# Optimization experiments

Hardware: AMD Instinct MI355X
Metric: run time of the kernel (lower is better)

Reference implementation:

```python
import jax, jax.numpy as jnp
import numpy as np

D_MODEL = 1024
N_HEADS = 16
D_FF = 4096
WINDOW = 256
EPS = 1e-5


def setup_inputs() -> dict:
    key = jax.random.key(0)
    ks = jax.random.split(key, 12)
    B, T, C = 4, 1024, D_MODEL
    s = lambda fan: 1.0 / np.sqrt(fan)
    return {
        "x": jax.random.normal(ks[0], (B, T, C), jnp.float32),
        "Wqkv": jax.random.normal(ks[1], (3 * C, C), jnp.float32) * s(C),
        "bqkv": jnp.zeros((3 * C,), jnp.float32),
        "Wo": jax.random.normal(ks[2], (C, C), jnp.float32) * s(C),
        "bo": jnp.zeros((C,), jnp.float32),
        "W1": jax.random.normal(ks[3], (D_FF, C), jnp.float32) * s(C),
        "b1": jnp.zeros((D_FF,), jnp.float32),
        "W2": jax.random.normal(ks[4], (C, D_FF), jnp.float32) * s(D_FF),
        "b2": jnp.zeros((C,), jnp.float32),
        "g1": jnp.ones((C,), jnp.float32),
        "be1": jnp.zeros((C,), jnp.float32),
        "g2": jnp.ones((C,), jnp.float32),
        "be2": jnp.zeros((C,), jnp.float32),
    }


def _layernorm(x, g, b):
    mu = jnp.mean(x, axis=-1, keepdims=True)
    var = jnp.mean(jnp.square(x - mu), axis=-1, keepdims=True)
    return (x - mu) * jax.lax.rsqrt(var + EPS) * g + b


def reference(x, Wqkv, bqkv, Wo, bo, W1, b1, W2, b2, g1, be1, g2, be2):
    B, T, C = x.shape
    H, Dh = N_HEADS, C // N_HEADS
    # QKV projection (torch MultiheadAttention packed in_proj)
    qkv = jnp.einsum("btc,ec->bte", x, Wqkv) + bqkv  # [B,T,3C]
    q, k, v = jnp.split(qkv, 3, axis=-1)
    q = q.reshape(B, T, H, Dh).transpose(0, 2, 1, 3)  # [B,H,T,Dh]
    k = k.reshape(B, T, H, Dh).transpose(0, 2, 1, 3)
    v = v.reshape(B, T, H, Dh).transpose(0, 2, 1, 3)
    scores = jnp.einsum("bhqd,bhkd->bhqk", q, k) / jnp.sqrt(jnp.float32(Dh))
    # causal banded mask: key j visible to query i iff 0 <= i-j < WINDOW
    i = jnp.arange(T)[:, None]
    j = jnp.arange(T)[None, :]
    band = (j <= i) & (i - j < WINDOW)
    scores = jnp.where(band, scores, -jnp.inf)
    attn = jax.nn.softmax(scores, axis=-1)
    ctx = jnp.einsum("bhqk,bhkd->bhqd", attn, v)  # [B,H,T,Dh]
    ctx = ctx.transpose(0, 2, 1, 3).reshape(B, T, C)
    attn_out = jnp.einsum("btc,oc->bto", ctx, Wo) + bo
    x = _layernorm(x + attn_out, g1, be1)
    h = jax.nn.gelu(jnp.einsum("btc,fc->btf", x, W1) + b1, approximate=False)
    ffn_out = jnp.einsum("btf,cf->btc", h, W2) + b2
    return _layernorm(x + ffn_out, g2, be2)
```

## Files before the change

kernel.cpp:

```cpp
#include <hip/hip_runtime.h>
#include <hip/hip_bf16.h>

typedef __attribute__((ext_vector_type(4))) float floatx4;
typedef __attribute__((ext_vector_type(8))) short shortx8;

struct bf4 { __hip_bfloat16 h[4]; };
union U8 { shortx8 v; __hip_bfloat16 h[8]; };
union U4 { unsigned long long v; __hip_bfloat16 h[4]; };

__device__ __forceinline__ void async_copy16(const __hip_bfloat16* g, __hip_bfloat16* l) {
  __builtin_amdgcn_global_load_lds((__attribute__((address_space(1))) void*)g,
                                   (__attribute__((address_space(3))) void*)l,
                                   16, 0, 0);
}

__global__ __launch_bounds__(256) void cast_all_kernel(
    const float* __restrict__ s0, __hip_bfloat16* __restrict__ d0, int nb0,
    const float* __restrict__ s1, __hip_bfloat16* __restrict__ d1, int nb1,
    const float* __restrict__ s2, __hip_bfloat16* __restrict__ d2, int nb2,
    const float* __restrict__ s3, __hip_bfloat16* __restrict__ d3, int nb3,
    const float* __restrict__ s4, __hip_bfloat16* __restrict__ d4) {
  int b = blockIdx.x;
  const float* src; __hip_bfloat16* dst;
  if (b < nb0) { src = s0; dst = d0; }
  else { b -= nb0;
    if (b < nb1) { src = s1; dst = d1; }
    else { b -= nb1;
      if (b < nb2) { src = s2; dst = d2; }
      else { b -= nb2;
        if (b < nb3) { src = s3; dst = d3; }
        else { b -= nb3; src = s4; dst = d4; }
      }
    }
  }
  const int i = b * 256 + threadIdx.x;
  const float4 v = ((const float4*)src)[i];
  bf4 o4;
  o4.h[0] = __float2bfloat16(v.x);
  o4.h[1] = __float2bfloat16(v.y);
  o4.h[2] = __float2bfloat16(v.z);
  o4.h[3] = __float2bfloat16(v.w);
  *(bf4*)(dst + (size_t)i * 4) = o4;
}

#define G6_VM(n)   asm volatile("s_waitcnt vmcnt(" #n ")" ::: "memory")
#define G6_BAR()   asm volatile("s_barrier" ::: "memory")
#define G6_LGKM0() asm volatile("s_waitcnt lgkmcnt(0)" ::: "memory")

#define G6_VMSEL(nf, np)                                                       \
  if (NBF == 4 || tid < 256 * NBF) { G6_VM(nf); } else { G6_VM(np); }

#define G6_BSTG(s, off)                                                        \
  if (NBF == 4 || tid < 256 * NBF) {                                           \
    async_copy16(Bg + (off), &Bs[(s) * BSLOT + tid * 8]);                      \
  }

#define G6_KLOOP()                                                             \
  async_copy16(Ag,      &As[0 * 8192 + tid * 8]);                              \
  G6_BSTG(0, 0)                                                                \
  async_copy16(Ag + 32, &As[1 * 8192 + tid * 8]);                              \
  G6_BSTG(1, 32)                                                               \
  async_copy16(Ag + 64, &As[2 * 8192 + tid * 8]);                              \
  G6_BSTG(2, 64)                                                               \
  G6_VMSEL(4, 2); G6_BAR();                                                    \
  {                                                                            \
    int rs = 0, ws = 3, koff = 96;                                             \
    for (int u = 0; u < NH; ++u) {                                             \
      const __hip_bfloat16* Asl = As + rs * 8192;                              \
      const __hip_bfloat16* Bsl = Bs + rs * BSLOT;                             \
      shortx8 fa[4], fb[NBF];                                                  \
      _Pragma("unroll")                                                        \
      for (int i_ = 0; i_ < 4; ++i_)                                           \
        fa[i_] = *(const shortx8*)&Asl[ard + i_ * 512];                        \
      _Pragma("unroll")                                                        \
      for (int i_ = 0; i_ < NBF; ++i_)                                         \
        fb[i_] = *(const shortx8*)&Bsl[brd + i_ * 512];                        \
      if (u + 3 < NH) {                                                        \
        async_copy16(Ag + koff, &As[ws * 8192 + tid * 8]);                     \
        G6_BSTG(ws, koff)                                                      \
        koff += 32;                                                            \
        G6_VMSEL(4, 2);                                                        \
      } else if (u + 2 < NH) { G6_VMSEL(2, 1); }                               \
      else if (u + 1 < NH)   { G6_VMSEL(0, 0); }                               \
      G6_BAR();                                                                \
      G6_LGKM0();                                                              \
      __builtin_amdgcn_s_setprio(1);                                           \
      _Pragma("unroll")                                                        \
      for (int mi_ = 0; mi_ < 4; ++mi_)                                        \
        _Pragma("unroll")                                                      \
        for (int ni_ = 0; ni_ < NBF; ++ni_)                                    \
          acc[mi_][ni_] = __builtin_amdgcn_mfma_f32_16x16x32_bf16(             \
              fa[mi_], fb[ni_], acc[mi_][ni_], 0, 0, 0);                       \
      __builtin_amdgcn_s_setprio(0);                                           \
      rs = (rs == 4) ? 0 : rs + 1;                                             \
      ws = (ws == 4) ? 0 : ws + 1;                                             \
    }                                                                          \
  }

template<int EPI, int NBF>
__global__ __launch_bounds__(1024, 4) void gemm256(
    const __hip_bfloat16* __restrict__ A,
    const __hip_bfloat16* __restrict__ B,
    const float* __restrict__ bias,
    __hip_bfloat16* __restrict__ outb,
    int M, int N, int K, int NT)
{
  __shared__ __align__(16) __hip_bfloat16 As[5 * 8192];
  __shared__ __align__(16) __hip_bfloat16 Bs[5 * 2048 * NBF];
  const int BSLOT = 2048 * NBF;
  const int tid  = threadIdx.x;
  const int lane = tid & 63;
  const int wave = tid >> 6;
  const int wr = wave >> 2;
  const int wc = wave & 3;
  const int fr = lane & 15;
  const int fq = lane >> 4;

  const int nwg = gridDim.x;
  const int cpx = nwg >> 3;
  const int swz = (blockIdx.x & 7) * cpx + (blockIdx.x >> 3);
  const int mt = swz / NT, nt = swz % NT;
  const long bm = (long)mt * 256, bn = (long)nt * (64 * NBF);

  const int srow = tid >> 2;
  const int sch  = (tid & 3) ^ ((tid >> 3) & 3);
  const __hip_bfloat16* Ag = A + (bm + srow) * (size_t)K + sch * 8;
  const __hip_bfloat16* Bg = B + (bn + srow) * (size_t)K + sch * 8;

  const int swc = (fq ^ ((fr >> 1) & 3)) << 3;
  const int ard = (wr * 64 + fr) * 32 + swc;
  const int brd = (wc * (16 * NBF) + fr) * 32 + swc;

  const floatx4 zero = {0.f, 0.f, 0.f, 0.f};
  floatx4 acc[4][NBF];
#pragma unroll
  for (int mi = 0; mi < 4; ++mi)
#pragma unroll
    for (int ni = 0; ni < NBF; ++ni) acc[mi][ni] = zero;

  const int NH = K >> 5;
  G6_KLOOP()

#pragma unroll
  for (int mi = 0; mi < 4; ++mi) {
#pragma unroll
    for (int ni = 0; ni < NBF; ++ni) {
      const long col = bn + wc * (16 * NBF) + ni * 16 + fr;
      const float bv = bias[col];
#pragma unroll
      for (int r = 0; r < 4; ++r) {
        const long row = bm + wr * 64 + mi * 16 + fq * 4 + r;
        float v = acc[mi][ni][r] + bv;
        if (EPI == 1) {
          const float u = v + 0.044715f * v * v * v;
          v = v / (1.0f + __expf(-1.5957691216057308f * u));
        }
        outb[(size_t)row * N + col] = __float2bfloat16(v);
      }
    }
  }
}

__global__ __launch_bounds__(1024, 4) void gemm256_splitk(
    const __hip_bfloat16* __restrict__ A,
    const __hip_bfloat16* __restrict__ B,
    __hip_bfloat16* __restrict__ part,
    int M, int N, int K, int Klen, int NT, int TPS)
{
  __shared__ __align__(16) __hip_bfloat16 As[5 * 8192];
  __shared__ __align__(16) __hip_bfloat16 Bs[5 * 8192];
  const int NBF = 4;
  const int BSLOT = 8192;
  const int tid  = threadIdx.x;
  const int lane = tid & 63;
  const int wave = tid >> 6;
  const int wr = wave >> 2;
  const int wc = wave & 3;
  const int fr = lane & 15;
  const int fq = lane >> 4;

  const int nwg = gridDim.x;
  const int cpx = nwg >> 3;
  const int swz = (blockIdx.x & 7) * cpx + (blockIdx.x >> 3);
  const int zt = swz / TPS;
  const int tile = swz % TPS;
  const int mt = tile / NT, nt = tile % NT;
  const long bm = (long)mt * 256, bn = (long)nt * 256;
  const int kstart = zt * Klen;

  const int srow = tid >> 2;
  const int sch  = (tid & 3) ^ ((tid >> 3) & 3);
  const __hip_bfloat16* Ag = A + (bm + srow) * (size_t)K + kstart + sch * 8;
  const __hip_bfloat16* Bg = B + (bn + srow) * (size_t)K + kstart + sch * 8;

  const int swc = (fq ^ ((fr >> 1) & 3)) << 3;
  const int ard = (wr * 64 + fr) * 32 + swc;
  const int brd = (wc * 64 + fr) * 32 + swc;

  const floatx4 zero = {0.f, 0.f, 0.f, 0.f};
  floatx4 acc[4][4];
#pragma unroll
  for (int mi = 0; mi < 4; ++mi)
#pragma unroll
    for (int ni = 0; ni < 4; ++ni) acc[mi][ni] = zero;

  const int NH = Klen >> 5;
  G6_KLOOP()

  __hip_bfloat16* outp = part + (size_t)zt * M * N;
#pragma unroll
  for (int mi = 0; mi < 4; ++mi) {
#pragma unroll
    for (int ni = 0; ni < 4; ++ni) {
      const long col = bn + wc * 64 + ni * 16 + fr;
#pragma unroll
      for (int r = 0; r < 4; ++r) {
        const long row = bm + wr * 64 + mi * 16 + fq * 4 + r;
        outp[(size_t)row * N + col] = __float2bfloat16(acc[mi][ni][r]);
      }
    }
  }
}

__global__ __launch_bounds__(256) void transpose_v_kernel(
    const __hip_bfloat16* __restrict__ qkv, __hip_bfloat16* __restrict__ vt)
{
  const int bh = blockIdx.y;
  const int tt = blockIdx.x;
  const int b = bh >> 4, h = bh & 15;
  __shared__ __hip_bfloat16 tile[64][65];
  const int tid = threadIdx.x;
  const int r = tid >> 2;
  const int c = (tid & 3) << 4;
  const __hip_bfloat16* src = qkv + (size_t)(b * 1024 + tt * 64 + r) * 3072 + 2048 + h * 64 + c;
  U8 u0, u1;
  u0.v = *(const shortx8*)src;
  u1.v = *(const shortx8*)(src + 8);
#pragma unroll
  for (int j = 0; j < 8; ++j) { tile[r][c + j] = u0.h[j]; tile[r][c + 8 + j] = u1.h[j]; }
  __syncthreads();
  U8 w0, w1;
#pragma unroll
  for (int j = 0; j < 8; ++j) { w0.h[j] = tile[c + j][r]; w1.h[j] = tile[c + 8 + j][r]; }
  __hip_bfloat16* dst = vt + ((size_t)bh * 64 + r) * 1024 + tt * 64 + c;
  *(shortx8*)dst       = w0.v;
  *(shortx8*)(dst + 8) = w1.v;
}

__global__ __launch_bounds__(256) void attn_kernel(
    const __hip_bfloat16* __restrict__ qkv,
    const __hip_bfloat16* __restrict__ vt,
    __hip_bfloat16* __restrict__ ctx)
{
  const int wave = threadIdx.x >> 6;
  const int lane = threadIdx.x & 63;
  const int gw = blockIdx.x * 4 + wave;
  const int qt = gw & 63;
  const int bh = gw >> 6;
  const int b = bh >> 4, h = bh & 15;
  const int fr = lane & 15, fq = lane >> 4;
  const int q0 = qt << 4;

  __shared__ __align__(16) __hip_bfloat16 Plds[4][16 * 32];
  __hip_bfloat16* Pw = Plds[wave];

  const __hip_bfloat16* qrow = qkv + (size_t)(b * 1024 + q0 + fr) * 3072 + h * 64;
  const shortx8 aq0 = *(const shortx8*)(qrow + fq * 8);
  const shortx8 aq1 = *(const shortx8*)(qrow + 32 + fq * 8);

  const float SC = 0.125f * 1.44269504088896f;
  float m_r[4] = {-1e30f, -1e30f, -1e30f, -1e30f};
  float l_r[4] = {0.f, 0.f, 0.f, 0.f};
  const floatx4 zero = {0.f, 0.f, 0.f, 0.f};
  floatx4 o[4];
#pragma unroll
  for (int nd = 0; nd < 4; ++nd) o[nd] = zero;

  const int kt0 = (q0 >= 255) ? ((q0 - 255) >> 5) : 0;
  const int kt1 = (q0 + 15) >> 5;
  for (int kt = kt0; kt <= kt1; ++kt) {
    const int kbase = kt << 5;
    const __hip_bfloat16* krow0 = qkv + (size_t)(b * 1024 + kbase + fr) * 3072 + 1024 + h * 64;
    const __hip_bfloat16* krow1 = krow0 + 16 * 3072;
    const shortx8 bk00 = *(const shortx8*)(krow0 + fq * 8);
    const shortx8 bk01 = *(const shortx8*)(krow0 + 32 + fq * 8);
    const shortx8 bk10 = *(const shortx8*)(krow1 + fq * 8);
    const shortx8 bk11 = *(const shortx8*)(krow1 + 32 + fq * 8);
    floatx4 s0 = zero, s1 = zero;
    s0 = __builtin_amdgcn_mfma_f32_16x16x32_bf16(aq0, bk00, s0, 0, 0, 0);
    s0 = __builtin_amdgcn_mfma_f32_16x16x32_bf16(aq1, bk01, s0, 0, 0, 0);
    s1 = __builtin_amdgcn_mfma_f32_16x16x32_bf16(aq0, bk10, s1, 0, 0, 0);
    s1 = __builtin_amdgcn_mfma_f32_16x16x32_bf16(aq1, bk11, s1, 0, 0, 0);
#pragma unroll
    for (int r = 0; r < 4; ++r) { s0[r] *= SC; s1[r] *= SC; }
    if (kbase + 31 > q0 || kbase < q0 - 240) {
#pragma unroll
      for (int r = 0; r < 4; ++r) {
        const int tq = q0 + fq * 4 + r;
        const int j0 = kbase + fr;
        const int j1 = j0 + 16;
        if (j0 > tq || j0 < tq - 255) s0[r] = -3e38f;
        if (j1 > tq || j1 < tq - 255) s1[r] = -3e38f;
      }
    }
#pragma unroll
    for (int r = 0; r < 4; ++r) {
      float vmax = fmaxf(s0[r], s1[r]);
      vmax = fmaxf(vmax, __shfl_xor(vmax, 1));
      vmax = fmaxf(vmax, __shfl_xor(vmax, 2));
      vmax = fmaxf(vmax, __shfl_xor(vmax, 4));
      vmax = fmaxf(vmax, __shfl_xor(vmax, 8));
      const float mnew = fmaxf(m_r[r], vmax);
      const float alpha = exp2f(m_r[r] - mnew);
      const float p0 = exp2f(s0[r] - mnew);
      const float p1 = exp2f(s1[r] - mnew);
      m_r[r] = mnew;
      float ps = p0 + p1;
      ps += __shfl_xor(ps, 1);
      ps += __shfl_xor(ps, 2);
      ps += __shfl_xor(ps, 4);
      ps += __shfl_xor(ps, 8);
      l_r[r] = l_r[r] * alpha + ps;
      o[0][r] *= alpha; o[1][r] *= alpha; o[2][r] *= alpha; o[3][r] *= alpha;
      Pw[(fq * 4 + r) * 32 + fr]      = __float2bfloat16(p0);
      Pw[(fq * 4 + r) * 32 + 16 + fr] = __float2bfloat16(p1);
    }
    asm volatile("s_waitcnt lgkmcnt(0)" ::: "memory");
    const shortx8 ap = *(const shortx8*)&Pw[fr * 32 + fq * 8];
#pragma unroll
    for (int nd = 0; nd < 4; ++nd) {
      const shortx8 bv = *(const shortx8*)&vt[((size_t)bh * 64 + nd * 16 + fr) * 1024 + kbase + fq * 8];
      o[nd] = __builtin_amdgcn_mfma_f32_16x16x32_bf16(ap, bv, o[nd], 0, 0, 0);
    }
    asm volatile("s_waitcnt lgkmcnt(0)" ::: "memory");
  }
#pragma unroll
  for (int nd = 0; nd < 4; ++nd)
#pragma unroll
    for (int r = 0; r < 4; ++r)
      ctx[(size_t)(b * 1024 + q0 + fq * 4 + r) * 1024 + h * 64 + nd * 16 + fr] =
          __float2bfloat16(o[nd][r] / l_r[r]);
}

template<int S, int WB>
__global__ __launch_bounds__(256) void ln_sum_kernel(
    const __hip_bfloat16* __restrict__ part,
    const float* __restrict__ resid,
    const float* __restrict__ bias,
    const float* __restrict__ g, const float* __restrict__ be,
    float* __restrict__ outf, __hip_bfloat16* __restrict__ outb)
{
  const int row = blockIdx.x;
  const int tid = threadIdx.x;
  const size_t base = (size_t)row * 1024;
  float4 v = ((const float4*)(resid + base))[tid];
  const float4 bv = ((const float4*)bias)[tid];
  v.x += bv.x; v.y += bv.y; v.z += bv.z; v.w += bv.w;
#pragma unroll
  for (int s = 0; s < S; ++s) {
    U4 p;
    p.v = *(const unsigned long long*)&part[(size_t)s * 4096 * 1024 + base + tid * 4];
    v.x += __bfloat162float(p.h[0]);
    v.y += __bfloat162float(p.h[1]);
    v.z += __bfloat162float(p.h[2]);
    v.w += __bfloat162float(p.h[3]);
  }
  float sm = v.x + v.y + v.z + v.w;
  float ss = v.x * v.x + v.y * v.y + v.z * v.z + v.w * v.w;
#pragma unroll
  for (int off = 1; off < 64; off <<= 1) {
    sm += __shfl_xor(sm, off);
    ss += __shfl_xor(ss, off);
  }
  __shared__ float red[8];
  if ((tid & 63) == 0) { red[tid >> 6] = sm; red[4 + (tid >> 6)] = ss; }
  __syncthreads();
  sm = red[0] + red[1] + red[2] + red[3];
  ss = red[4] + red[5] + red[6] + red[7];
  const float mu = sm * (1.0f / 1024.0f);
  const float rs = rsqrtf(ss * (1.0f / 1024.0f) - mu * mu + 1e-5f);
  const float4 gg = ((const float4*)g)[tid];
  const float4 bb = ((const float4*)be)[tid];
  float4 y;
  y.x = (v.x - mu) * rs * gg.x + bb.x;
  y.y = (v.y - mu) * rs * gg.y + bb.y;
  y.z = (v.z - mu) * rs * gg.z + bb.z;
  y.w = (v.w - mu) * rs * gg.w + bb.w;
  ((float4*)(outf + base))[tid] = y;
  if (WB) {
    bf4 o4;
    o4.h[0] = __float2bfloat16(y.x);
    o4.h[1] = __float2bfloat16(y.y);
    o4.h[2] = __float2bfloat16(y.z);
    o4.h[3] = __float2bfloat16(y.w);
    *(bf4*)(outb + base + tid * 4) = o4;
  }
}

extern "C" void kernel_launch(void* const* d_in, const int* in_sizes, int n_in,
                              void* d_out, int out_size, void* d_ws, size_t ws_size,
                              hipStream_t stream) {
  const float* x    = (const float*)d_in[0];
  const float* Wqkv = (const float*)d_in[1];
  const float* bqkv = (const float*)d_in[2];
  const float* Wo   = (const float*)d_in[3];
  const float* bo   = (const float*)d_in[4];
  const float* W1   = (const float*)d_in[5];
  const float* b1   = (const float*)d_in[6];
  const float* W2   = (const float*)d_in[7];
  const float* b2   = (const float*)d_in[8];
  const float* g1   = (const float*)d_in[9];
  const float* be1  = (const float*)d_in[10];
  const float* g2   = (const float*)d_in[11];
  const float* be2  = (const float*)d_in[12];

  char* ws = (char*)d_ws;
  size_t off = 0;
  auto alloc = [&](size_t bytes) -> void* {
    void* p = ws + off;
    off += (bytes + 255) & ~(size_t)255;
    return p;
  };
  __hip_bfloat16* wqkvb = (__hip_bfloat16*)alloc(6291456);
  __hip_bfloat16* wob   = (__hip_bfloat16*)alloc(2097152);
  __hip_bfloat16* w1b   = (__hip_bfloat16*)alloc(8388608);
  __hip_bfloat16* w2b   = (__hip_bfloat16*)alloc(8388608);
  __hip_bfloat16* xb    = (__hip_bfloat16*)alloc(8388608);
  __hip_bfloat16* qkvb  = (__hip_bfloat16*)alloc(25165824);
  __hip_bfloat16* vtb   = (__hip_bfloat16*)alloc(8388608);
  __hip_bfloat16* ctxb  = (__hip_bfloat16*)alloc(8388608);
  __hip_bfloat16* part  = (__hip_bfloat16*)alloc(4u * 8388608);
  float*          x1f   = (float*)alloc(16777216);
  __hip_bfloat16* x1b   = (__hip_bfloat16*)alloc(8388608);
  __hip_bfloat16* hb    = (__hip_bfloat16*)alloc(33554432);
  (void)ws_size; (void)in_sizes; (void)n_in; (void)out_size;

  cast_all_kernel<<<16384, 256, 0, stream>>>(x, xb, 4096,
                                             Wqkv, wqkvb, 3072,
                                             Wo, wob, 1024,
                                             W1, w1b, 4096,
                                             W2, w2b);
  gemm256<0, 3><<<256, 1024, 0, stream>>>(xb, wqkvb, bqkv, qkvb, 4096, 3072, 1024, 16);
  transpose_v_kernel<<<dim3(16, 64), 256, 0, stream>>>(qkvb, vtb);
  attn_kernel<<<1024, 256, 0, stream>>>(qkvb, vtb, ctxb);
  gemm256_splitk<<<256, 1024, 0, stream>>>(ctxb, wob, part, 4096, 1024, 1024, 256, 4, 64);
  ln_sum_kernel<4, 1><<<4096, 256, 0, stream>>>(part, x, bo, g1, be1, x1f, x1b);
  gemm256<1, 4><<<256, 1024, 0, stream>>>(x1b, w1b, b1, hb, 4096, 4096, 1024, 16);
  gemm256_splitk<<<256, 1024, 0, stream>>>(hb, w2b, part, 4096, 1024, 4096, 1024, 4, 64);
  ln_sum_kernel<4, 0><<<4096, 256, 0, stream>>>(part, x1f, b2, g2, be2, (float*)d_out, nullptr);
}
```

Baseline: 323.1 us.

## Software-pipeline K loads and hoist V loads in banded attention loop

The attention loop is manually unrolled by two with ping-pong K register sets, so the next K tile is prefetched while the current tile runs softmax. V fragments are loaded at the top of each step instead of after the P tile is written, so their latency hides behind the QK MFMAs and softmax. The P staging buffer row stride goes from 32 to 40 elements to reduce LDS bank conflicts. In exchange the kernel uses more registers, which may lower occupancy.

```diff
diff --git a/kernel.cpp b/kernel.cpp
--- a/kernel.cpp
+++ b/kernel.cpp
@@ -247,6 +247,74 @@
   *(shortx8*)(dst + 8) = w1.v;
 }
 
+#define ATTN_LOADK(k0, k1, k2, k3, ktv)                                        \
+  {                                                                            \
+    const __hip_bfloat16* kr0_ =                                               \
+        qkv + (size_t)(b * 1024 + ((ktv) << 5) + fr) * 3072 + 1024 + h * 64;   \
+    const __hip_bfloat16* kr1_ = kr0_ + 16 * 3072;                             \
+    k0 = *(const shortx8*)(kr0_ + fq * 8);                                     \
+    k1 = *(const shortx8*)(kr0_ + 32 + fq * 8);                                \
+    k2 = *(const shortx8*)(kr1_ + fq * 8);                                     \
+    k3 = *(const shortx8*)(kr1_ + 32 + fq * 8);                                \
+  }
+
+#define ATTN_STEP(KC0, KC1, KC2, KC3, KN0, KN1, KN2, KN3, ktv, PREF)           \
+  {                                                                            \
+    const int kbase = (ktv) << 5;                                              \
+    const __hip_bfloat16* vrow_ =                                              \
+        vt + ((size_t)bh * 64 + fr) * 1024 + kbase + fq * 8;                   \
+    const shortx8 vv0 = *(const shortx8*)(vrow_);                              \
+    const shortx8 vv1 = *(const shortx8*)(vrow_ + 16 * 1024);                  \
+    const shortx8 vv2 = *(const shortx8*)(vrow_ + 32 * 1024);                  \
+    const shortx8 vv3 = *(const shortx8*)(vrow_ + 48 * 1024);                  \
+    floatx4 s0 = zero, s1 = zero;                                              \
+    s0 = __builtin_amdgcn_mfma_f32_16x16x32_bf16(aq0, KC0, s0, 0, 0, 0);       \
+    s0 = __builtin_amdgcn_mfma_f32_16x16x32_bf16(aq1, KC1, s0, 0, 0, 0);       \
+    s1 = __builtin_amdgcn_mfma_f32_16x16x32_bf16(aq0, KC2, s1, 0, 0, 0);       \
+    s1 = __builtin_amdgcn_mfma_f32_16x16x32_bf16(aq1, KC3, s1, 0, 0, 0);       \
+    if (PREF) ATTN_LOADK(KN0, KN1, KN2, KN3, (ktv) + 1)                        \
+    _Pragma("unroll")                                                          \
+    for (int r = 0; r < 4; ++r) { s0[r] *= SC; s1[r] *= SC; }                  \
+    if (kbase + 31 > q0 || kbase < q0 - 240) {                                 \
+      _Pragma("unroll")                                                        \
+      for (int r = 0; r < 4; ++r) {                                            \
+        const int tq = q0 + fq * 4 + r;                                        \
+        const int j0 = kbase + fr;                                             \
+        const int j1 = j0 + 16;                                                \
+        if (j0 > tq || j0 < tq - 255) s0[r] = -3e38f;                          \
+        if (j1 > tq || j1 < tq - 255) s1[r] = -3e38f;                          \
+      }                                                                        \
+    }                                                                          \
+    _Pragma("unroll")                                                          \
+    for (int r = 0; r < 4; ++r) {                                              \
+      float vmax = fmaxf(s0[r], s1[r]);                                        \
+      vmax = fmaxf(vmax, __shfl_xor(vmax, 1));                                 \
+      vmax = fmaxf(vmax, __shfl_xor(vmax, 2));                                 \
+      vmax = fmaxf(vmax, __shfl_xor(vmax, 4));                                 \
+      vmax = fmaxf(vmax, __shfl_xor(vmax, 8));                                 \
+      const float mnew = fmaxf(m_r[r], vmax);                                  \
+      const float alpha = exp2f(m_r[r] - mnew);                                \
+      const float p0 = exp2f(s0[r] - mnew);                                    \
+      const float p1 = exp2f(s1[r] - mnew);                                    \
+      m_r[r] = mnew;                                                           \
+      float ps = p0 + p1;                                                      \
+      ps += __shfl_xor(ps, 1);                                                 \
+      ps += __shfl_xor(ps, 2);                                                 \
+      ps += __shfl_xor(ps, 4);                                                 \
+      ps += __shfl_xor(ps, 8);                                                 \
+      l_r[r] = l_r[r] * alpha + ps;                                            \
+      o[0][r] *= alpha; o[1][r] *= alpha; o[2][r] *= alpha; o[3][r] *= alpha;  \
+      Pw[(fq * 4 + r) * 40 + fr]      = __float2bfloat16(p0);                  \
+      Pw[(fq * 4 + r) * 40 + 16 + fr] = __float2bfloat16(p1);                  \
+    }                                                                          \
+    asm volatile("s_waitcnt lgkmcnt(0)" ::: "memory");                         \
+    const shortx8 ap = *(const shortx8*)&Pw[fr * 40 + fq * 8];                 \
+    o[0] = __builtin_amdgcn_mfma_f32_16x16x32_bf16(ap, vv0, o[0], 0, 0, 0);    \
+    o[1] = __builtin_amdgcn_mfma_f32_16x16x32_bf16(ap, vv1, o[1], 0, 0, 0);    \
+    o[2] = __builtin_amdgcn_mfma_f32_16x16x32_bf16(ap, vv2, o[2], 0, 0, 0);    \
+    o[3] = __builtin_amdgcn_mfma_f32_16x16x32_bf16(ap, vv3, o[3], 0, 0, 0);    \
+  }
+
 __global__ __launch_bounds__(256) void attn_kernel(
     const __hip_bfloat16* __restrict__ qkv,
     const __hip_bfloat16* __restrict__ vt,
@@ -261,7 +329,7 @@
   const int fr = lane & 15, fq = lane >> 4;
   const int q0 = qt << 4;
 
-  __shared__ __align__(16) __hip_bfloat16 Plds[4][16 * 32];
+  __shared__ __align__(16) __hip_bfloat16 Plds[4][16 * 40];
   __hip_bfloat16* Pw = Plds[wave];
 
   const __hip_bfloat16* qrow = qkv + (size_t)(b * 1024 + q0 + fr) * 3072 + h * 64;
@@ -278,62 +346,21 @@
 
   const int kt0 = (q0 >= 255) ? ((q0 - 255) >> 5) : 0;
   const int kt1 = (q0 + 15) >> 5;
-  for (int kt = kt0; kt <= kt1; ++kt) {
-    const int kbase = kt << 5;
-    const __hip_bfloat16* krow0 = qkv + (size_t)(b * 1024 + kbase + fr) * 3072 + 1024 + h * 64;
-    const __hip_bfloat16* krow1 = krow0 + 16 * 3072;
-    const shortx8 bk00 = *(const shortx8*)(krow0 + fq * 8);
-    const shortx8 bk01 = *(const shortx8*)(krow0 + 32 + fq * 8);
-    const shortx8 bk10 = *(const shortx8*)(krow1 + fq * 8);
-    const shortx8 bk11 = *(const shortx8*)(krow1 + 32 + fq * 8);
-    floatx4 s0 = zero, s1 = zero;
-    s0 = __builtin_amdgcn_mfma_f32_16x16x32_bf16(aq0, bk00, s0, 0, 0, 0);
-    s0 = __builtin_amdgcn_mfma_f32_16x16x32_bf16(aq1, bk01, s0, 0, 0, 0);
-    s1 = __builtin_amdgcn_mfma_f32_16x16x32_bf16(aq0, bk10, s1, 0, 0, 0);
-    s1 = __builtin_amdgcn_mfma_f32_16x16x32_bf16(aq1, bk11, s1, 0, 0, 0);
-#pragma unroll
-    for (int r = 0; r < 4; ++r) { s0[r] *= SC; s1[r] *= SC; }
-    if (kbase + 31 > q0 || kbase < q0 - 240) {
-#pragma unroll
-      for (int r = 0; r < 4; ++r) {
-        const int tq = q0 + fq * 4 + r;
-        const int j0 = kbase + fr;
-        const int j1 = j0 + 16;
-        if (j0 > tq || j0 < tq - 255) s0[r] = -3e38f;
-        if (j1 > tq || j1 < tq - 255) s1[r] = -3e38f;
-      }
-    }
-#pragma unroll
-    for (int r = 0; r < 4; ++r) {
-      float vmax = fmaxf(s0[r], s1[r]);
-      vmax = fmaxf(vmax, __shfl_xor(vmax, 1));
-      vmax = fmaxf(vmax, __shfl_xor(vmax, 2));
-      vmax = fmaxf(vmax, __shfl_xor(vmax, 4));
-      vmax = fmaxf(vmax, __shfl_xor(vmax, 8));
-      const float mnew = fmaxf(m_r[r], vmax);
-      const float alpha = exp2f(m_r[r] - mnew);
-      const float p0 = exp2f(s0[r] - mnew);
-      const float p1 = exp2f(s1[r] - mnew);
-      m_r[r] = mnew;
-      float ps = p0 + p1;
-      ps += __shfl_xor(ps, 1);
-      ps += __shfl_xor(ps, 2);
-      ps += __shfl_xor(ps, 4);
-      ps += __shfl_xor(ps, 8);
-      l_r[r] = l_r[r] * alpha + ps;
-      o[0][r] *= alpha; o[1][r] *= alpha; o[2][r] *= alpha; o[3][r] *= alpha;
-      Pw[(fq * 4 + r) * 32 + fr]      = __float2bfloat16(p0);
-      Pw[(fq * 4 + r) * 32 + 16 + fr] = __float2bfloat16(p1);
-    }
-    asm volatile("s_waitcnt lgkmcnt(0)" ::: "memory");
-    const shortx8 ap = *(const shortx8*)&Pw[fr * 32 + fq * 8];
-#pragma unroll
-    for (int nd = 0; nd < 4; ++nd) {
-      const shortx8 bv = *(const shortx8*)&vt[((size_t)bh * 64 + nd * 16 + fr) * 1024 + kbase + fq * 8];
-      o[nd] = __builtin_amdgcn_mfma_f32_16x16x32_bf16(ap, bv, o[nd], 0, 0, 0);
-    }
-    asm volatile("s_waitcnt lgkmcnt(0)" ::: "memory");
-  }
+
+  shortx8 ka0, ka1, ka2, ka3, kb0, kb1, kb2, kb3;
+  ATTN_LOADK(ka0, ka1, ka2, ka3, kt0)
+  int kt = kt0;
+  for (;;) {
+    const bool more1 = kt < kt1;
+    ATTN_STEP(ka0, ka1, ka2, ka3, kb0, kb1, kb2, kb3, kt, more1)
+    if (!more1) break;
+    ++kt;
+    const bool more2 = kt < kt1;
+    ATTN_STEP(kb0, kb1, kb2, kb3, ka0, ka1, ka2, ka3, kt, more2)
+    if (!more2) break;
+    ++kt;
+  }
+
 #pragma unroll
   for (int nd = 0; nd < 4; ++nd)
 #pragma unroll
```

New measurement: 319.7 us. About the same (-1.0%).
